# Kernel tuning notes

Measured on AMD Instinct MI355X. Metric: run time of the kernel, lower is better.

Reference implementation:

```python
import jax, jax.numpy as jnp
import numpy as np

N_NODES = 131072
D = 256            # nfeat_dim
E = 262144         # edges per graph (pos and neg)
IN_DIM = 2 * D     # 512
HID = IN_DIM // 2  # 256


def setup_inputs() -> dict:
    key = jax.random.key(0)
    k0, k1, k2, k3, k4, k5, k6 = jax.random.split(key, 7)
    block_outputs = jax.random.normal(k0, (N_NODES, D), dtype=jnp.float32)
    pos_src = jax.random.randint(k1, (E,), 0, N_NODES)
    pos_dst = jax.random.randint(k2, (E,), 0, N_NODES)
    neg_src = jax.random.randint(k3, (E,), 0, N_NODES)
    neg_dst = jax.random.randint(k4, (E,), 0, N_NODES)
    # LinkPredLayer params (xavier-normal-like init for weights)
    w1_std = float(np.sqrt(2.0 / (IN_DIM + HID)))
    w2_std = float(np.sqrt(2.0 / (HID + 1)))
    W1 = jax.random.normal(k5, (IN_DIM, HID), dtype=jnp.float32) * w1_std
    b1 = jnp.zeros((HID,), dtype=jnp.float32)
    W2 = jax.random.normal(k6, (HID, 1), dtype=jnp.float32) * w2_std
    b2 = jnp.zeros((1,), dtype=jnp.float32)
    return {"block_outputs": block_outputs, "pos_src": pos_src, "pos_dst": pos_dst,
            "neg_src": neg_src, "neg_dst": neg_dst,
            "W1": W1, "b1": b1, "W2": W2, "b2": b2}


def _linkpred_mlp(h, W1, b1, W2, b2):
    # eval mode: dropout = identity; BatchNorm defined in __init__ but unused in forward
    h = jax.nn.relu(h @ W1 + b1)        # [E_total, HID]
    return jax.nn.sigmoid(h @ W2 + b2)  # [E_total, 1]


def reference(block_outputs, pos_src, pos_dst, neg_src, neg_dst, W1, b1, W2, b2):
    # edge gather: src || dst concat per edge (apply_edges(linkpred_concat))
    pos_emb = jnp.concatenate([block_outputs[pos_src], block_outputs[pos_dst]], axis=1)  # [E, 2D]
    neg_emb = jnp.concatenate([block_outputs[neg_src], block_outputs[neg_dst]], axis=1)  # [E, 2D]
    emb = jnp.concatenate([pos_emb, neg_emb], axis=0)  # [2E, 2D]
    logits = _linkpred_mlp(emb, W1, b1, W2, b2)        # [2E, 1]
    labels = jnp.zeros_like(logits).at[:pos_emb.shape[0]].set(1.0)
    return logits.squeeze(-1), labels.squeeze(-1)
```

## Files before the change

### kernel.cpp

```cpp
#include <hip/hip_runtime.h>
#include <hip/hip_bf16.h>
#include <stdint.h>

#define E_EDGES 262144
#define DFEAT 256
#define KDIM 512
#define NNODES 131072

typedef __attribute__((ext_vector_type(8))) short short8;
typedef __attribute__((ext_vector_type(4))) float f32x4;

static __device__ __forceinline__ unsigned f2bf(float x) {
    unsigned u = __float_as_uint(x);
    u += 0x7fffu + ((u >> 16) & 1u);
    return u >> 16;
}
static __device__ __forceinline__ float bf2f(unsigned short s) {
    return __uint_as_float(((unsigned)s) << 16);
}

__global__ __launch_bounds__(256) void prep_wB2_kernel(const float* __restrict__ W1,
                                                       unsigned short* __restrict__ wB2) {
    int idx = blockIdx.x * 256 + threadIdx.x;
    int n = idx >> 8;
    int k = idx & 255;
    int srow = k + ((n >= 256) ? 256 : 0);
    wB2[((size_t)(k >> 3) * 512 + n) * 8 + (k & 7)] = (unsigned short)f2bf(W1[srow * 256 + (n & 255)]);
}

__global__ __launch_bounds__(512, 2) void gemm_uv5_kernel(const float* __restrict__ table,
                                                          const unsigned short* __restrict__ wB2,
                                                          unsigned short* __restrict__ uv) {
    __shared__ __align__(16) unsigned char lds[65536];

    const int tid = threadIdx.x;
    const int l = tid & 63;
    const int wv = tid >> 6;
    const int l15 = l & 15;
    const int lq = l >> 4;

    short8 bfr[8][4];
#pragma unroll
    for (int kk = 0; kk < 8; ++kk)
#pragma unroll
        for (int j = 0; j < 4; ++j) {
            int col = wv * 64 + j * 16 + l15;
            bfr[kk][j] = *(const short8*)(wB2 + ((size_t)(kk * 4 + lq) * 512 + col) * 8);
        }

    const int srow = tid >> 4;
    const int gc0 = (tid & 15) * 2;
    const int tile0 = blockIdx.x * 8;

    float4 sreg[4];
    auto loadA = [&](int t) {
        const float* src = table + (size_t)(tile0 + t) * 32 * DFEAT + (size_t)srow * DFEAT;
#pragma unroll
        for (int m = 0; m < 2; ++m) {
            sreg[m * 2]     = *(const float4*)(src + (gc0 + m) * 8);
            sreg[m * 2 + 1] = *(const float4*)(src + (gc0 + m) * 8 + 4);
        }
    };
    auto writeA = [&](int buf) {
        unsigned char* base = lds + buf * 16384 + srow * 512;
#pragma unroll
        for (int m = 0; m < 2; ++m) {
            int gc = gc0 + m;
            uint4 w;
            w.x = f2bf(sreg[m * 2].x)     | (f2bf(sreg[m * 2].y) << 16);
            w.y = f2bf(sreg[m * 2].z)     | (f2bf(sreg[m * 2].w) << 16);
            w.z = f2bf(sreg[m * 2 + 1].x) | (f2bf(sreg[m * 2 + 1].y) << 16);
            w.w = f2bf(sreg[m * 2 + 1].z) | (f2bf(sreg[m * 2 + 1].w) << 16);
            int phys = (gc & 16) | ((gc ^ (srow & 15)) & 15);
            *(uint4*)(base + phys * 16) = w;
        }
    };

    loadA(0);
    writeA(0);
    asm volatile("s_waitcnt lgkmcnt(0)" ::: "memory");
    __builtin_amdgcn_s_barrier();

    for (int t = 0; t < 8; ++t) {
        const int m0 = (tile0 + t) * 32;

        if (t < 7) loadA(t + 1);

        f32x4 acc[2][4];
#pragma unroll
        for (int i = 0; i < 2; ++i)
#pragma unroll
            for (int j = 0; j < 4; ++j)
                acc[i][j] = (f32x4){0.f, 0.f, 0.f, 0.f};

        const unsigned char* Ab = lds + (t & 1) * 16384;
#pragma unroll
        for (int kk = 0; kk < 8; ++kk) {
            int g = kk * 4 + lq;
            int phys = (g & 16) | ((g ^ l15) & 15);
            short8 af[2];
#pragma unroll
            for (int i = 0; i < 2; ++i)
                af[i] = *(const short8*)(Ab + (i * 16 + l15) * 512 + phys * 16);
#pragma unroll
            for (int i = 0; i < 2; ++i)
#pragma unroll
                for (int j = 0; j < 4; ++j)
                    acc[i][j] = __builtin_amdgcn_mfma_f32_16x16x32_bf16(bfr[kk][j], af[i], acc[i][j], 0, 0, 0);
        }

        unsigned char* Bnc = lds + 32768;
#pragma unroll
        for (int i = 0; i < 2; ++i)
#pragma unroll
            for (int j = 0; j < 4; ++j) {
                unsigned lo = f2bf(acc[i][j][0]) | (f2bf(acc[i][j][1]) << 16);
                unsigned hi = f2bf(acc[i][j][2]) | (f2bf(acc[i][j][3]) << 16);
                int nodep = i * 16 + l15;
                int colbyte = wv * 128 + j * 32 + lq * 8;
                int g = colbyte >> 4;
                int phys = (g & ~15) | ((g ^ nodep) & 15);
                *(uint2*)(Bnc + nodep * 1024 + phys * 16 + (colbyte & 15)) = make_uint2(lo, hi);
            }

        asm volatile("s_waitcnt lgkmcnt(0)" ::: "memory");
        __builtin_amdgcn_s_barrier();

#pragma unroll
        for (int p = 0; p < 4; ++p) {
            int node = p * 8 + (tid >> 6);
            int col16 = tid & 63;
            int phys = (col16 & ~15) | ((col16 ^ node) & 15);
            uint4 w = *(const uint4*)(Bnc + node * 1024 + phys * 16);
            *(uint4*)(uv + ((size_t)(m0 + node)) * 512 + col16 * 8) = w;
        }

        if (t < 7) writeA((t + 1) & 1);

        asm volatile("s_waitcnt lgkmcnt(0)" ::: "memory");
        __builtin_amdgcn_s_barrier();
    }
}

__global__ __launch_bounds__(256) void edge2_kernel(
    const unsigned short* __restrict__ uv,
    const int* __restrict__ pos_src, const int* __restrict__ pos_dst,
    const int* __restrict__ neg_src, const int* __restrict__ neg_dst,
    const float* __restrict__ b1, const float* __restrict__ W2,
    const float* __restrict__ b2,
    float* __restrict__ out) {

    const int tid = threadIdx.x;
    const int m = tid & 31;
    const int hw = tid >> 5;
    const int eb = blockIdx.x * 64;
    const int e0 = eb + hw * 8;
    const bool is_pos = (eb < E_EDGES);
    const int ee0 = is_pos ? e0 : e0 - E_EDGES;
    const int* __restrict__ srcp = is_pos ? pos_src : neg_src;
    const int* __restrict__ dstp = is_pos ? pos_dst : neg_dst;

    int4 sa = *(const int4*)(srcp + ee0);
    int4 sb = *(const int4*)(srcp + ee0 + 4);
    int4 da = *(const int4*)(dstp + ee0);
    int4 db = *(const int4*)(dstp + ee0 + 4);
    const int sidx[8] = {sa.x, sa.y, sa.z, sa.w, sb.x, sb.y, sb.z, sb.w};
    const int didx[8] = {da.x, da.y, da.z, da.w, db.x, db.y, db.z, db.w};

    short8 uvec[8], vvec[8];
#pragma unroll
    for (int j = 0; j < 8; ++j) {
        uvec[j] = *(const short8*)(uv + (size_t)sidx[j] * 512 + m * 8);
        vvec[j] = *(const short8*)(uv + (size_t)didx[j] * 512 + 256 + m * 8);
    }

    float b1a[8], w2a[8];
    *(float4*)&b1a[0] = *(const float4*)(b1 + m * 8);
    *(float4*)&b1a[4] = *(const float4*)(b1 + m * 8 + 4);
    *(float4*)&w2a[0] = *(const float4*)(W2 + m * 8);
    *(float4*)&w2a[4] = *(const float4*)(W2 + m * 8 + 4);
    const float b2v = b2[0];

    float p[8];
#pragma unroll
    for (int j = 0; j < 8; ++j) {
        float pp = 0.f;
#pragma unroll
        for (int i = 0; i < 8; ++i) {
            float z = bf2f((unsigned short)uvec[j][i]) + bf2f((unsigned short)vvec[j][i]) + b1a[i];
            z = fmaxf(z, 0.f);
            pp = fmaf(z, w2a[i], pp);
        }
#pragma unroll
        for (int mk = 1; mk < 32; mk <<= 1) pp += __shfl_xor(pp, mk, 64);
        p[j] = pp;
    }

    float pj = p[0];
#pragma unroll
    for (int k = 1; k < 8; ++k) if (m == k) pj = p[k];
    if (m < 8) {
        float x = pj + b2v;
        out[(size_t)e0 + m] = 1.0f / (1.0f + __expf(-x));
    }
    if (tid < 64)
        out[(size_t)(2 * E_EDGES) + eb + tid] = is_pos ? 1.0f : 0.0f;
}

__global__ __launch_bounds__(256) void conv_table_kernel(const float* __restrict__ t,
                                                         unsigned short* __restrict__ o) {
    int idx = blockIdx.x * 256 + threadIdx.x;
    float4 a = ((const float4*)t)[idx * 2];
    float4 b = ((const float4*)t)[idx * 2 + 1];
    uint4 w;
    w.x = f2bf(a.x) | (f2bf(a.y) << 16);
    w.y = f2bf(a.z) | (f2bf(a.w) << 16);
    w.z = f2bf(b.x) | (f2bf(b.y) << 16);
    w.w = f2bf(b.z) | (f2bf(b.w) << 16);
    ((uint4*)o)[idx] = w;
}

__global__ __launch_bounds__(256) void prep_w1t_kernel(const float* __restrict__ W1,
                                                       unsigned short* __restrict__ w1t) {
    int idx = blockIdx.x * 256 + threadIdx.x;
    int k = idx >> 8;
    int n = idx & 255;
    w1t[n * KDIM + k] = (unsigned short)f2bf(W1[idx]);
}

__global__ __launch_bounds__(256) void linkpred4_kernel(
    const unsigned short* __restrict__ tblb,
    const int* __restrict__ pos_src, const int* __restrict__ pos_dst,
    const int* __restrict__ neg_src, const int* __restrict__ neg_dst,
    const float* __restrict__ b1, const float* __restrict__ W2,
    const float* __restrict__ b2,
    const unsigned short* __restrict__ w1t,
    float* __restrict__ out) {

    __shared__ __align__(16) unsigned short Bs[64 * 512];

    const int tid = threadIdx.x;
    const int l = tid & 63;
    const int wv = tid >> 6;
    const int l15 = l & 15;
    const int lq = l >> 4;
    const int m0 = blockIdx.x * 128;
    const bool is_pos = (m0 < E_EDGES);

    int nsrc[2], ndst[2];
#pragma unroll
    for (int mt = 0; mt < 2; ++mt) {
        int m = m0 + wv * 32 + mt * 16 + l15;
        if (is_pos) { nsrc[mt] = pos_src[m];            ndst[mt] = pos_dst[m]; }
        else        { int mm = m - E_EDGES; nsrc[mt] = neg_src[mm]; ndst[mt] = neg_dst[mm]; }
    }

    auto stageB = [&](int c) {
#pragma unroll
        for (int i = 0; i < 16; ++i) {
            int lc = wv * 16 + i;
            int gc = c * 64 + lc;
            const unsigned short* g = w1t + (size_t)gc * KDIM + ((l ^ i) << 3);
            char* lp = (char*)Bs + lc * 1024;
            __builtin_amdgcn_global_load_lds(
                (const __attribute__((address_space(1))) void*)g,
                (__attribute__((address_space(3))) void*)lp, 16, 0, 0);
        }
    };

    stageB(0);
    __builtin_amdgcn_sched_barrier(0);

    short8 af[2][16];
#pragma unroll
    for (int h = 0; h < 16; ++h)
#pragma unroll
        for (int mt = 0; mt < 2; ++mt) {
            int node = (h < 8) ? nsrc[mt] : ndst[mt];
            const unsigned short* g = tblb + (size_t)node * DFEAT + (h & 7) * 32 + lq * 8;
            af[mt][h] = *(const short8*)g;
        }
    __builtin_amdgcn_sched_barrier(0);

    f32x4 acc[2][4];
#pragma unroll
    for (int mt = 0; mt < 2; ++mt)
#pragma unroll
        for (int j = 0; j < 4; ++j)
            acc[mt][j] = (f32x4){0.f, 0.f, 0.f, 0.f};
    float rowacc[2][4] = {{0.f, 0.f, 0.f, 0.f}, {0.f, 0.f, 0.f, 0.f}};

    const char* Bb = (const char*)Bs;

#pragma unroll
    for (int c = 0; c < 4; ++c) {
        if (c == 0) {
            asm volatile("s_waitcnt vmcnt(32)" ::: "memory");
        } else {
            __syncthreads();
            stageB(c);
#pragma unroll
            for (int mt = 0; mt < 2; ++mt)
#pragma unroll
                for (int j = 0; j < 4; ++j) {
                    int col = (c - 1) * 64 + j * 16 + l15;
                    float b1v = b1[col], w2v = W2[col];
#pragma unroll
                    for (int r = 0; r < 4; ++r) {
                        float hv = fmaxf(acc[mt][j][r] + b1v, 0.f);
                        rowacc[mt][r] = fmaf(hv, w2v, rowacc[mt][r]);
                    }
                    acc[mt][j] = (f32x4){0.f, 0.f, 0.f, 0.f};
                }
            asm volatile("s_waitcnt vmcnt(0)" ::: "memory");
        }
        __builtin_amdgcn_s_barrier();

        __builtin_amdgcn_s_setprio(1);
#pragma unroll
        for (int h = 0; h < 16; ++h) {
            short8 bf[4];
#pragma unroll
            for (int j = 0; j < 4; ++j) {
                int cl = j * 16 + l15;
                int phys = (h * 4 + lq) ^ l15;
                bf[j] = *(const short8*)(Bb + cl * 1024 + phys * 16);
            }
#pragma unroll
            for (int mt = 0; mt < 2; ++mt)
#pragma unroll
                for (int j = 0; j < 4; ++j)
                    acc[mt][j] = __builtin_amdgcn_mfma_f32_16x16x32_bf16(af[mt][h], bf[j], acc[mt][j], 0, 0, 0);
        }
        __builtin_amdgcn_s_setprio(0);
    }

#pragma unroll
    for (int mt = 0; mt < 2; ++mt)
#pragma unroll
        for (int j = 0; j < 4; ++j) {
            int col = 3 * 64 + j * 16 + l15;
            float b1v = b1[col], w2v = W2[col];
#pragma unroll
            for (int r = 0; r < 4; ++r) {
                float hv = fmaxf(acc[mt][j][r] + b1v, 0.f);
                rowacc[mt][r] = fmaf(hv, w2v, rowacc[mt][r]);
            }
        }

    const float b2v = b2[0];
#pragma unroll
    for (int mt = 0; mt < 2; ++mt)
#pragma unroll
        for (int r = 0; r < 4; ++r) {
            float p = rowacc[mt][r];
#pragma unroll
            for (int mk = 1; mk < 16; mk <<= 1) p += __shfl_xor(p, mk, 64);
            if (l15 == 0) {
                int m = m0 + wv * 32 + mt * 16 + lq * 4 + r;
                float sg = 1.0f / (1.0f + __expf(-(p + b2v)));
                out[(size_t)m] = sg;
                out[(size_t)(2 * E_EDGES) + m] = is_pos ? 1.0f : 0.0f;
            }
        }
}

__global__ __launch_bounds__(256) void linkpred_fb_kernel(
    const float* __restrict__ table,
    const int* __restrict__ pos_src, const int* __restrict__ pos_dst,
    const int* __restrict__ neg_src, const int* __restrict__ neg_dst,
    const float* __restrict__ b1, const float* __restrict__ W2,
    const float* __restrict__ b2,
    const unsigned short* __restrict__ w1t,
    float* __restrict__ out) {

    __shared__ __align__(16) unsigned short As[2][64 * 64];
    __shared__ int sIdx[64], dIdx[64];
    __shared__ float wpart[4][64];

    const int tid = threadIdx.x;
    const int l = tid & 63;
    const int wv = tid >> 6;
    const int m0 = blockIdx.x * 64;

    if (tid < 64) {
        int m = m0 + tid;
        int si, di;
        if (m < E_EDGES) { si = pos_src[m];            di = pos_dst[m]; }
        else             { si = neg_src[m - E_EDGES];  di = neg_dst[m - E_EDGES]; }
        sIdx[tid] = si;
        dIdx[tid] = di;
    }

    float b1v[4], w2v[4];
#pragma unroll
    for (int j = 0; j < 4; j++) {
        int n = wv * 64 + j * 16 + (l & 15);
        b1v[j] = b1[n];
        w2v[j] = W2[n];
    }

    __syncthreads();

    const int e0 = tid >> 3;
    const int q  = tid & 7;
    const int e1 = e0 + 32;

    auto pack_write = [&](int buf, int e, const float4& x, const float4& y) {
        uint4 w;
        w.x = f2bf(x.x) | (f2bf(x.y) << 16);
        w.y = f2bf(x.z) | (f2bf(x.w) << 16);
        w.z = f2bf(y.x) | (f2bf(y.y) << 16);
        w.w = f2bf(y.z) | (f2bf(y.w) << 16);
        int byte = e * 128 + q * 16;
        byte ^= (e & 7) << 4;
        *(uint4*)((char*)(&As[buf][0]) + byte) = w;
    };

    {
        const float* p0 = table + (size_t)sIdx[e0] * DFEAT + q * 8;
        const float* p1 = table + (size_t)sIdx[e1] * DFEAT + q * 8;
        float4 a0 = *(const float4*)p0, a1 = *(const float4*)(p0 + 4);
        float4 c0 = *(const float4*)p1, c1 = *(const float4*)(p1 + 4);
        pack_write(0, e0, a0, a1);
        pack_write(0, e1, c0, c1);
    }
    __syncthreads();

    f32x4 acc[4][4];
#pragma unroll
    for (int i = 0; i < 4; i++)
#pragma unroll
        for (int j = 0; j < 4; j++)
            acc[i][j] = (f32x4){0.f, 0.f, 0.f, 0.f};

    for (int s = 0; s < 8; s++) {
        float4 a0, a1, c0, c1;
        if (s < 7) {
            int sn = s + 1;
            const int* idxA = (sn < 4) ? sIdx : dIdx;
            int cb = (sn & 3) * 64 + q * 8;
            const float* p0 = table + (size_t)idxA[e0] * DFEAT + cb;
            const float* p1 = table + (size_t)idxA[e1] * DFEAT + cb;
            a0 = *(const float4*)p0; a1 = *(const float4*)(p0 + 4);
            c0 = *(const float4*)p1; c1 = *(const float4*)(p1 + 4);
        }

        const int cur = s & 1;
        const char* Abase = (const char*)(&As[cur][0]);
#pragma unroll
        for (int h = 0; h < 2; h++) {
            short8 af[4], bf[4];
#pragma unroll
            for (int i = 0; i < 4; i++) {
                int row = i * 16 + (l & 15);
                int byte = row * 128 + h * 64 + ((l >> 4) << 4);
                byte ^= (l & 7) << 4;
                af[i] = *(const short8*)(Abase + byte);
            }
#pragma unroll
            for (int j = 0; j < 4; j++) {
                int col = wv * 64 + j * 16 + (l & 15);
                int koff = s * 64 + h * 32 + ((l >> 4) << 3);
                bf[j] = *(const short8*)(w1t + col * KDIM + koff);
            }
#pragma unroll
            for (int i = 0; i < 4; i++)
#pragma unroll
                for (int j = 0; j < 4; j++)
                    acc[i][j] = __builtin_amdgcn_mfma_f32_16x16x32_bf16(af[i], bf[j], acc[i][j], 0, 0, 0);
        }

        if (s < 7) {
            pack_write((s + 1) & 1, e0, a0, a1);
            pack_write((s + 1) & 1, e1, c0, c1);
        }
        __syncthreads();
    }

    float part[16];
#pragma unroll
    for (int i = 0; i < 4; i++) {
#pragma unroll
        for (int r = 0; r < 4; r++) {
            float p = 0.f;
#pragma unroll
            for (int j = 0; j < 4; j++) {
                float hv = acc[i][j][r] + b1v[j];
                hv = fmaxf(hv, 0.f);
                p = fmaf(hv, w2v[j], p);
            }
#pragma unroll
            for (int mk = 1; mk < 16; mk <<= 1) p += __shfl_xor(p, mk, 64);
            part[i * 4 + r] = p;
        }
    }
    if ((l & 15) == 0) {
        int g = l >> 4;
#pragma unroll
        for (int i = 0; i < 4; i++)
#pragma unroll
            for (int r = 0; r < 4; r++)
                wpart[wv][i * 16 + g * 4 + r] = part[i * 4 + r];
    }
    __syncthreads();

    if (tid < 64) {
        float x = wpart[0][tid] + wpart[1][tid] + wpart[2][tid] + wpart[3][tid] + b2[0];
        float sg = 1.0f / (1.0f + __expf(-x));
        out[(size_t)m0 + tid] = sg;
        out[(size_t)(2 * E_EDGES) + m0 + tid] = (m0 < E_EDGES) ? 1.0f : 0.0f;
    }
}

extern "C" void kernel_launch(void* const* d_in, const int* in_sizes, int n_in,
                              void* d_out, int out_size, void* d_ws, size_t ws_size,
                              hipStream_t stream) {
    const float* table = (const float*)d_in[0];
    const int* ps = (const int*)d_in[1];
    const int* pd = (const int*)d_in[2];
    const int* ns = (const int*)d_in[3];
    const int* nd = (const int*)d_in[4];
    const float* W1 = (const float*)d_in[5];
    const float* b1 = (const float*)d_in[6];
    const float* W2 = (const float*)d_in[7];
    const float* b2 = (const float*)d_in[8];
    float* out = (float*)d_out;

    const size_t wB_bytes  = (size_t)KDIM * 256 * 2;
    const size_t uv_bytes  = (size_t)NNODES * KDIM * 2;
    const size_t tbl_bytes = (size_t)NNODES * DFEAT * 2;
    const size_t w1t_bytes = (size_t)256 * KDIM * 2;

    if (ws_size >= wB_bytes + uv_bytes) {
        unsigned short* wB2 = (unsigned short*)d_ws;
        unsigned short* uv = (unsigned short*)((char*)d_ws + wB_bytes);
        hipLaunchKernelGGL(prep_wB2_kernel, dim3(512), dim3(256), 0, stream, W1, wB2);
        hipLaunchKernelGGL(gemm_uv5_kernel, dim3(512), dim3(512), 0, stream, table, wB2, uv);
        hipLaunchKernelGGL(edge2_kernel, dim3(8192), dim3(256), 0, stream,
                           uv, ps, pd, ns, nd, b1, W2, b2, out);
    } else if (ws_size >= tbl_bytes + w1t_bytes) {
        unsigned short* tblb = (unsigned short*)d_ws;
        unsigned short* w1t = (unsigned short*)((char*)d_ws + tbl_bytes);
        hipLaunchKernelGGL(conv_table_kernel, dim3(16384), dim3(256), 0, stream, table, tblb);
        hipLaunchKernelGGL(prep_w1t_kernel, dim3(512), dim3(256), 0, stream, W1, w1t);
        hipLaunchKernelGGL(linkpred4_kernel, dim3(4096), dim3(256), 0, stream,
                           tblb, ps, pd, ns, nd, b1, W2, b2, w1t, out);
    } else {
        unsigned short* w1t = (unsigned short*)d_ws;
        hipLaunchKernelGGL(prep_w1t_kernel, dim3(512), dim3(256), 0, stream, W1, w1t);
        hipLaunchKernelGGL(linkpred_fb_kernel, dim3(8192), dim3(256), 0, stream,
                           table, ps, pd, ns, nd, b1, W2, b2, w1t, out);
    }
}
```

Baseline: 140.7 us.

## Split node-projection GEMM output columns across two blocks with per-wave epilogue staging

The node-projection GEMM now gives each block one 256-column half of the output, so twice as many blocks each keep half the B fragments and accumulators in registers. The epilogue stages results in a private per-wave LDS slice instead of a shared block buffer, which removes one barrier per tile. LDS drops to 48KB and launch bounds ask for 4 blocks per CU to raise occupancy. Table loads become nontemporal and the MFMA loop raises wave priority. The cost is that every fp32 table tile is now loaded and converted twice, once per column half, and the uv stores become narrower 64-byte row segments.

```diff
diff --git a/kernel.cpp b/kernel.cpp
--- a/kernel.cpp
+++ b/kernel.cpp
@@ -17,6 +17,9 @@
 }
 static __device__ __forceinline__ float bf2f(unsigned short s) {
     return __uint_as_float(((unsigned)s) << 16);
+}
+static __device__ __forceinline__ f32x4 nt_load4(const float* p) {
+    return __builtin_nontemporal_load((const f32x4*)p);
 }
 
 __global__ __launch_bounds__(256) void prep_wB2_kernel(const float* __restrict__ W1,
@@ -28,37 +31,39 @@
     wB2[((size_t)(k >> 3) * 512 + n) * 8 + (k & 7)] = (unsigned short)f2bf(W1[srow * 256 + (n & 255)]);
 }
 
-__global__ __launch_bounds__(512, 2) void gemm_uv5_kernel(const float* __restrict__ table,
+__global__ __launch_bounds__(512, 4) void gemm_uv7_kernel(const float* __restrict__ table,
                                                           const unsigned short* __restrict__ wB2,
                                                           unsigned short* __restrict__ uv) {
-    __shared__ __align__(16) unsigned char lds[65536];
+    __shared__ __align__(16) unsigned char lds[49152];
 
     const int tid = threadIdx.x;
     const int l = tid & 63;
     const int wv = tid >> 6;
     const int l15 = l & 15;
     const int lq = l >> 4;
-
-    short8 bfr[8][4];
+    const int flavor = blockIdx.x & 1;
+    const int mt0 = (blockIdx.x >> 1) * 8;
+
+    short8 bfr[8][2];
 #pragma unroll
     for (int kk = 0; kk < 8; ++kk)
 #pragma unroll
-        for (int j = 0; j < 4; ++j) {
-            int col = wv * 64 + j * 16 + l15;
+        for (int j = 0; j < 2; ++j) {
+            int col = flavor * 256 + wv * 32 + j * 16 + l15;
             bfr[kk][j] = *(const short8*)(wB2 + ((size_t)(kk * 4 + lq) * 512 + col) * 8);
         }
 
     const int srow = tid >> 4;
     const int gc0 = (tid & 15) * 2;
-    const int tile0 = blockIdx.x * 8;
-
-    float4 sreg[4];
+    unsigned char* const slice = lds + 32768 + wv * 2048;
+
+    f32x4 sreg[4];
     auto loadA = [&](int t) {
-        const float* src = table + (size_t)(tile0 + t) * 32 * DFEAT + (size_t)srow * DFEAT;
+        const float* src = table + (size_t)(mt0 + t) * 32 * DFEAT + (size_t)srow * DFEAT;
 #pragma unroll
         for (int m = 0; m < 2; ++m) {
-            sreg[m * 2]     = *(const float4*)(src + (gc0 + m) * 8);
-            sreg[m * 2 + 1] = *(const float4*)(src + (gc0 + m) * 8 + 4);
+            sreg[m * 2]     = nt_load4(src + (gc0 + m) * 8);
+            sreg[m * 2 + 1] = nt_load4(src + (gc0 + m) * 8 + 4);
         }
     };
     auto writeA = [&](int buf) {
@@ -67,10 +72,10 @@
         for (int m = 0; m < 2; ++m) {
             int gc = gc0 + m;
             uint4 w;
-            w.x = f2bf(sreg[m * 2].x)     | (f2bf(sreg[m * 2].y) << 16);
-            w.y = f2bf(sreg[m * 2].z)     | (f2bf(sreg[m * 2].w) << 16);
-            w.z = f2bf(sreg[m * 2 + 1].x) | (f2bf(sreg[m * 2 + 1].y) << 16);
-            w.w = f2bf(sreg[m * 2 + 1].z) | (f2bf(sreg[m * 2 + 1].w) << 16);
+            w.x = f2bf(sreg[m * 2][0])     | (f2bf(sreg[m * 2][1]) << 16);
+            w.y = f2bf(sreg[m * 2][2])     | (f2bf(sreg[m * 2][3]) << 16);
+            w.z = f2bf(sreg[m * 2 + 1][0]) | (f2bf(sreg[m * 2 + 1][1]) << 16);
+            w.w = f2bf(sreg[m * 2 + 1][2]) | (f2bf(sreg[m * 2 + 1][3]) << 16);
             int phys = (gc & 16) | ((gc ^ (srow & 15)) & 15);
             *(uint4*)(base + phys * 16) = w;
         }
@@ -82,18 +87,19 @@
     __builtin_amdgcn_s_barrier();
 
     for (int t = 0; t < 8; ++t) {
-        const int m0 = (tile0 + t) * 32;
+        const int m0 = (mt0 + t) * 32;
 
         if (t < 7) loadA(t + 1);
 
-        f32x4 acc[2][4];
+        f32x4 acc[2][2];
 #pragma unroll
         for (int i = 0; i < 2; ++i)
 #pragma unroll
-            for (int j = 0; j < 4; ++j)
+            for (int j = 0; j < 2; ++j)
                 acc[i][j] = (f32x4){0.f, 0.f, 0.f, 0.f};
 
         const unsigned char* Ab = lds + (t & 1) * 16384;
+        __builtin_amdgcn_s_setprio(1);
 #pragma unroll
         for (int kk = 0; kk < 8; ++kk) {
             int g = kk * 4 + lq;
@@ -105,34 +111,29 @@
 #pragma unroll
             for (int i = 0; i < 2; ++i)
 #pragma unroll
-                for (int j = 0; j < 4; ++j)
+                for (int j = 0; j < 2; ++j)
                     acc[i][j] = __builtin_amdgcn_mfma_f32_16x16x32_bf16(bfr[kk][j], af[i], acc[i][j], 0, 0, 0);
         }
-
-        unsigned char* Bnc = lds + 32768;
+        __builtin_amdgcn_s_setprio(0);
+
 #pragma unroll
         for (int i = 0; i < 2; ++i)
 #pragma unroll
-            for (int j = 0; j < 4; ++j) {
+            for (int j = 0; j < 2; ++j) {
+                int n = i * 16 + l15;
+                int s = j * 4 + lq;
                 unsigned lo = f2bf(acc[i][j][0]) | (f2bf(acc[i][j][1]) << 16);
                 unsigned hi = f2bf(acc[i][j][2]) | (f2bf(acc[i][j][3]) << 16);
-                int nodep = i * 16 + l15;
-                int colbyte = wv * 128 + j * 32 + lq * 8;
-                int g = colbyte >> 4;
-                int phys = (g & ~15) | ((g ^ nodep) & 15);
-                *(uint2*)(Bnc + nodep * 1024 + phys * 16 + (colbyte & 15)) = make_uint2(lo, hi);
-            }
-
-        asm volatile("s_waitcnt lgkmcnt(0)" ::: "memory");
-        __builtin_amdgcn_s_barrier();
-
-#pragma unroll
-        for (int p = 0; p < 4; ++p) {
-            int node = p * 8 + (tid >> 6);
-            int col16 = tid & 63;
-            int phys = (col16 & ~15) | ((col16 ^ node) & 15);
-            uint4 w = *(const uint4*)(Bnc + node * 1024 + phys * 16);
-            *(uint4*)(uv + ((size_t)(m0 + node)) * 512 + col16 * 8) = w;
+                *(uint2*)(slice + n * 64 + ((s ^ (n & 6)) * 8)) = make_uint2(lo, hi);
+            }
+#pragma unroll
+        for (int r = 0; r < 2; ++r) {
+            int u_ = r * 64 + l;
+            int n = u_ >> 2;
+            int sub = u_ & 3;
+            int phys = (2 * sub) ^ (n & 6);
+            uint4 w = *(const uint4*)(slice + n * 64 + phys * 8);
+            *(uint4*)(uv + ((size_t)(m0 + n)) * 512 + flavor * 256 + wv * 32 + sub * 8) = w;
         }
 
         if (t < 7) writeA((t + 1) & 1);
@@ -536,7 +537,7 @@
         unsigned short* wB2 = (unsigned short*)d_ws;
         unsigned short* uv = (unsigned short*)((char*)d_ws + wB_bytes);
         hipLaunchKernelGGL(prep_wB2_kernel, dim3(512), dim3(256), 0, stream, W1, wB2);
-        hipLaunchKernelGGL(gemm_uv5_kernel, dim3(512), dim3(512), 0, stream, table, wB2, uv);
+        hipLaunchKernelGGL(gemm_uv7_kernel, dim3(1024), dim3(512), 0, stream, table, wB2, uv);
         hipLaunchKernelGGL(edge2_kernel, dim3(8192), dim3(256), 0, stream,
                            uv, ps, pd, ns, nd, b1, W2, b2, out);
     } else if (ws_size >= tbl_bytes + w1t_bytes) {
```

Result: slower. 186.2 us (+32.4%).
